# Performance work log

Hardware: AMD Instinct MI355X
Metric: run time of the kernel (lower is better)

The kernel has to match this reference:

```python
import jax, jax.numpy as jnp
import numpy as np

BLOCK_SIZE = 16
NVFP4_LEVELS = np.array([0.0, 0.5, 1.0, 1.5, 2.0, 3.0, 4.0, 6.0], dtype=np.float32)


def quantize_to_nvfp4(x, block_size=BLOCK_SIZE):
    """NVFP4 fake-quant: per-16-element block, scale = amax/6, round |x| to nearest level."""
    levels = jnp.asarray(NVFP4_LEVELS, dtype=x.dtype)
    orig_shape = x.shape
    xf = x.reshape(-1, block_size)                                   # [nblk, 16]
    amax = jnp.clip(jnp.max(jnp.abs(xf), axis=-1, keepdims=True), 1e-12)
    scale = amax / 6.0                                               # [nblk, 1]
    x_norm = jnp.abs(xf) / scale                                     # in [0, 6]
    idx = jnp.argmin(jnp.abs(x_norm[..., None] - levels), axis=-1)   # nearest level (first on ties, like torch)
    x_q = jnp.sign(xf) * levels[idx] * scale
    return x_q.reshape(orig_shape)


def _magnitude_mask_2_4(w):
    # keep 2 largest-|.| of every group of 4 along in_features (row-wise 2:4)
    out_f, in_f = w.shape
    a = jnp.abs(w).reshape(out_f, in_f // 4, 4)
    thr = jnp.sort(a, axis=-1)[..., 2:3]          # 2nd-largest magnitude in group
    mask = (a >= thr).reshape(out_f, in_f)
    return mask.astype(w.dtype)


def setup_inputs() -> dict:
    key = jax.random.key(0)
    k_x, k_w, k_s, k_a, k_b, k_bias = jax.random.split(key, 6)
    B, S, IN_F, OUT_F, RANK = 2, 2048, 4096, 4096, 32
    x = jax.random.normal(k_x, (B, S, IN_F), dtype=jnp.float32)
    smooth_scale = jax.random.uniform(k_s, (IN_F,), dtype=jnp.float32, minval=0.5, maxval=2.0)
    # realistic calibrated weight: 2:4 magnitude-sparse then NVFP4 fake-quantized
    w = jax.random.normal(k_w, (OUT_F, IN_F), dtype=jnp.float32) * 0.02
    w_sparse = w * _magnitude_mask_2_4(w)
    w_quantized = quantize_to_nvfp4(w_sparse)
    lora_a = jax.random.normal(k_a, (RANK, IN_F), dtype=jnp.float32) * 0.02
    lora_b = jax.random.normal(k_b, (OUT_F, RANK), dtype=jnp.float32) * 0.02
    bias = jax.random.normal(k_bias, (OUT_F,), dtype=jnp.float32)
    return {"x": x, "smooth_scale": smooth_scale, "w_quantized": w_quantized,
            "lora_a": lora_a, "lora_b": lora_b, "bias": bias}


def reference(x, smooth_scale, w_quantized, lora_a, lora_b, bias):
    # x: [B, S, IN], smooth_scale: [IN], w_quantized: [OUT, IN]
    x_smoothed = x * smooth_scale                                    # SmoothQuant activation scaling
    x_q = quantize_to_nvfp4(x_smoothed, BLOCK_SIZE)                  # block fake-quant of activations
    base_out = jnp.einsum('bsi,oi->bso', x_q, w_quantized)           # 2:4-sparse quantized matmul
    svd_out = jnp.einsum('bsr,or->bso',
                         jnp.einsum('bsi,ri->bsr', x_smoothed, lora_a), lora_b)  # low-rank correction
    return base_out + svd_out + bias
```

## Files before the change

kernel.cpp:

```cpp
#include <hip/hip_runtime.h>
#include <hip/hip_bf16.h>
#include <stdint.h>

typedef __attribute__((ext_vector_type(8)))  __bf16 bf16x8;
typedef __attribute__((ext_vector_type(4)))  float  f32x4;
typedef __attribute__((ext_vector_type(16))) float  f32x16;

#define KP 4160

__device__ inline void async_copy16(const void* g, void* l) {
  __builtin_amdgcn_global_load_lds((const __attribute__((address_space(1))) void*)g,
                                   (__attribute__((address_space(3))) void*)l, 16, 0, 0);
}

__global__ __launch_bounds__(256) void prep_kernel(
    const float* __restrict__ x, const float* __restrict__ ss,
    const float* __restrict__ w, const float* __restrict__ la,
    const float* __restrict__ lb, __bf16* __restrict__ Ab,
    __bf16* __restrict__ Bb) {
  __shared__ float red[4][16][32];
  int b   = blockIdx.x;
  int tid = threadIdx.x;

  if (b < 2048) {
    int m0 = (b >> 3) << 4;
    int by = b & 7;
    int row = m0 + (tid >> 4);
    int cb0 = tid & 15;
#pragma unroll
    for (int i = 0; i < 2; i++) {
      int col = (by << 9) + ((cb0 + (i << 4)) << 4);
      const float4* xp = (const float4*)(x + ((size_t)row << 12) + col);
      const float4* sp = (const float4*)(ss + col);
      float xs[16];
#pragma unroll
      for (int j = 0; j < 4; j++) {
        float4 xv = xp[j]; float4 sv = sp[j];
        xs[4*j+0] = xv.x * sv.x; xs[4*j+1] = xv.y * sv.y;
        xs[4*j+2] = xv.z * sv.z; xs[4*j+3] = xv.w * sv.w;
      }
      float amax = 0.f;
#pragma unroll
      for (int j = 0; j < 16; j++) amax = fmaxf(amax, fabsf(xs[j]));
      amax = fmaxf(amax, 1e-12f);
      float scale = amax / 6.0f;
      bf16x8 o0, o1;
#pragma unroll
      for (int j = 0; j < 16; j++) {
        float a  = fabsf(xs[j]);
        float xn = a / scale;
        float lvl;
        if (xn < 2.25f) {
          lvl = 0.5f * __builtin_ceilf(__builtin_fmaf(2.0f, xn, -0.5f));
        } else {
          lvl = (xn <= 2.5f) ? 2.0f : (xn <= 3.5f) ? 3.0f
              : (xn <= 5.0f) ? 4.0f : 6.0f;
        }
        float mag = lvl * scale;
        float q = (xs[j] > 0.f) ? mag : ((xs[j] < 0.f) ? -mag : 0.f);
        if (j < 8) o0[j] = (__bf16)q; else o1[j-8] = (__bf16)q;
      }
      __bf16* dst = Ab + (size_t)row * KP + col;
      *(bf16x8*)dst = o0;
      *(bf16x8*)(dst + 8) = o1;
    }
  } else if (b < 10368) {
    int id  = (b - 2048) * 256 + tid;
    int row = id / 520;
    int g   = id - row * 520;
    bf16x8 v;
    if (g < 512) {
      const float4* wp = (const float4*)(w + ((size_t)row << 12) + (g << 3));
      float4 a = wp[0], bb = wp[1];
      v[0]=(__bf16)a.x;  v[1]=(__bf16)a.y;  v[2]=(__bf16)a.z;  v[3]=(__bf16)a.w;
      v[4]=(__bf16)bb.x; v[5]=(__bf16)bb.y; v[6]=(__bf16)bb.z; v[7]=(__bf16)bb.w;
    } else if (g < 516) {
      const float* p = lb + (size_t)row * 32 + ((g - 512) << 3);
#pragma unroll
      for (int j = 0; j < 8; j++) v[j] = (__bf16)p[j];
    } else {
#pragma unroll
      for (int j = 0; j < 8; j++) v[j] = (__bf16)0.f;
    }
    *(bf16x8*)(Bb + (size_t)row * KP + ((size_t)g << 3)) = v;
  } else {
    int j16  = (b - 10368) << 4;
    int wave = tid >> 6, lane = tid & 63;
    int lrow = lane & 15, kg = lane >> 4;
    f32x4 acc0 = {0.f,0.f,0.f,0.f}, acc1 = {0.f,0.f,0.f,0.f};
    const float* xrow = x + ((size_t)(j16 + lrow) << 12);
    const float* a0   = la + ((size_t)lrow << 12);
    const float* a1   = a0 + (16 << 12);
#pragma unroll 4
    for (int k0 = 0; k0 < 32; k0++) {
      int kk = (wave << 10) + (k0 << 5) + (kg << 3);
      float xv[8], sv[8], v0[8], v1[8];
      *(float4*)&xv[0] = *(const float4*)(xrow + kk);
      *(float4*)&xv[4] = *(const float4*)(xrow + kk + 4);
      *(float4*)&sv[0] = *(const float4*)(ss + kk);
      *(float4*)&sv[4] = *(const float4*)(ss + kk + 4);
      *(float4*)&v0[0] = *(const float4*)(a0 + kk);
      *(float4*)&v0[4] = *(const float4*)(a0 + kk + 4);
      *(float4*)&v1[0] = *(const float4*)(a1 + kk);
      *(float4*)&v1[4] = *(const float4*)(a1 + kk + 4);
      bf16x8 af, b0, b1;
#pragma unroll
      for (int q = 0; q < 8; q++) {
        af[q] = (__bf16)(xv[q] * sv[q]);
        b0[q] = (__bf16)v0[q];
        b1[q] = (__bf16)v1[q];
      }
      acc0 = __builtin_amdgcn_mfma_f32_16x16x32_bf16(af, b0, acc0, 0, 0, 0);
      acc1 = __builtin_amdgcn_mfma_f32_16x16x32_bf16(af, b1, acc1, 0, 0, 0);
    }
#pragma unroll
    for (int r = 0; r < 4; r++) {
      red[wave][kg*4 + r][lrow]      = acc0[r];
      red[wave][kg*4 + r][16 + lrow] = acc1[r];
    }
    __syncthreads();
    for (int o = tid; o < 512; o += 256) {
      int rr = o >> 5, cc = o & 31;
      float s = red[0][rr][cc] + red[1][rr][cc] + red[2][rr][cc] + red[3][rr][cc];
      __bf16* dst = Ab + (size_t)(j16 + rr) * KP + 4096;
      dst[cc]      = (__bf16)s;
      dst[32 + cc] = (__bf16)0.f;
    }
  }
}

#define GBAR() __builtin_amdgcn_s_barrier()
#define PRI1() __builtin_amdgcn_s_setprio(1)
#define PRI0() __builtin_amdgcn_s_setprio(0)
#define WVM(n) asm volatile("s_waitcnt vmcnt(" #n ")" ::: "memory")

#define STG(srcb, dstb, bb, h, t) do {                                         \
    const __bf16* _s = (srcb) + (size_t)(h) * (128 * (size_t)KP)               \
                              + ((size_t)(t) << 6);                            \
    char* _d = (dstb) + ((bb) << 15) + ((h) << 14);                            \
    async_copy16(_s, _d);                                                      \
    async_copy16(_s + 32, _d + 1024);                                          \
  } while (0)

#define KOFF(KS) ((((KS) >> 1) << 10) + ((((KS) & 1) << 5) ^ sx))

#define RD_A(base, KS) do { _Pragma("unroll")                                  \
  for (int mf = 0; mf < 4; mf++)                                               \
    af[mf] = *(const bf16x8*)((base) + (mf << 12) + KOFF(KS)); } while (0)

#define RD_B(base, KS) do {                                                    \
    Br[0*4 + (KS)] = *(const bf16x8*)((base) + KOFF(KS));                      \
    Br[1*4 + (KS)] = *(const bf16x8*)((base) + 4096 + KOFF(KS)); } while (0)

#define MM8(KS) do { _Pragma("unroll")                                         \
  for (int mf = 0; mf < 4; mf++) _Pragma("unroll")                             \
  for (int nf = 0; nf < 2; nf++)                                               \
    acc[mf][nf] = __builtin_amdgcn_mfma_f32_32x32x16_bf16(                     \
        af[mf], Br[nf*4 + (KS)], acc[mf][nf], 0, 0, 0); } while (0)

__global__ __launch_bounds__(512, 2) void gemm_kernel(const __bf16* __restrict__ A,
                                                      const __bf16* __restrict__ B,
                                                      const float* __restrict__ bias,
                                                      float* __restrict__ C) {
  extern __shared__ char lds[];
  const int tid  = threadIdx.x;
  const int w    = tid >> 6, lane = tid & 63;
  const int ln31 = lane & 31, kg2 = lane >> 5;
  const int wm   = w >> 2, wn = w & 3;
  const int bid  = blockIdx.x;
  const int sbid = ((bid & 7) << 5) | (bid >> 3);
  const int bm   = sbid >> 4, bn = sbid & 15;
  const size_t m0 = (size_t)bm << 8, n0 = (size_t)bn << 8;

  const int rr = (w << 4) + (lane >> 2);
  const int kk = ((lane & 3) ^ (((lane >> 5) & 1) << 1)) << 3;
  const __bf16* aS = A + (m0 + rr) * (size_t)KP + kk;
  const __bf16* bS = B + (n0 + rr) * (size_t)KP + kk;
  char* dA = lds + (w << 11);
  char* dB = lds + 65536 + (w << 11);

  const int sx = (lane & 8) << 2;
  const int cA = ((ln31 >> 4) << 11) + ((ln31 & 15) << 6) + (kg2 << 4);
  const int cB = ((((wn & 1) << 2) + (ln31 >> 4)) << 11)
               + ((ln31 & 15) << 6) + (kg2 << 4);
  const char* pA0 = lds + (wm << 14) + cA;
  const char* pA1 = pA0 + 32768;
  const char* pB0 = lds + 65536 + ((wn >> 1) << 14) + cB;
  const char* pB1 = pB0 + 32768;

  bf16x8 af[4], Br[8];
  f32x16 acc[4][2];
#pragma unroll
  for (int i = 0; i < 4; i++)
#pragma unroll
    for (int j = 0; j < 2; j++)
#pragma unroll
      for (int q = 0; q < 16; q++) acc[i][j][q] = 0.f;

  STG(bS, dB, 0, 0, 0); STG(bS, dB, 0, 1, 0);
  STG(aS, dA, 0, 0, 0); STG(aS, dA, 0, 1, 0);
  STG(bS, dB, 1, 0, 1); STG(bS, dB, 1, 1, 1);
  WVM(4);
  GBAR();

#pragma unroll 1
  for (int i = 0; i < 32; i++) {
    const int t1 = 2*i + 1, t2 = 2*i + 2;
    int t3 = 2*i + 3; if (t3 > 64) t3 = 64;
    STG(aS, dA, 1, 0, t1);
    RD_B(pB0, 0); RD_B(pB0, 1); RD_A(pA0, 0);
    PRI1(); MM8(0); PRI0();
    GBAR();
    STG(aS, dA, 1, 1, t1);
    RD_B(pB0, 2); RD_B(pB0, 3); RD_A(pA0, 1);
    PRI1(); MM8(1); PRI0();
    GBAR();
    STG(bS, dB, 0, 0, t2);
    RD_A(pA0, 2);
    PRI1(); MM8(2); PRI0();
    GBAR();
    STG(bS, dB, 0, 1, t2);
    RD_A(pA0, 3);
    PRI1(); MM8(3); PRI0();
    WVM(4);
    GBAR();
    STG(aS, dA, 0, 0, t2);
    RD_B(pB1, 0); RD_B(pB1, 1); RD_A(pA1, 0);
    PRI1(); MM8(0); PRI0();
    GBAR();
    STG(aS, dA, 0, 1, t2);
    RD_B(pB1, 2); RD_B(pB1, 3); RD_A(pA1, 1);
    PRI1(); MM8(1); PRI0();
    GBAR();
    STG(bS, dB, 1, 0, t3);
    RD_A(pA1, 2);
    PRI1(); MM8(2); PRI0();
    GBAR();
    STG(bS, dB, 1, 1, t3);
    RD_A(pA1, 3);
    PRI1(); MM8(3); PRI0();
    WVM(4);
    GBAR();
  }

  RD_B(pB0, 0); RD_B(pB0, 1); RD_B(pB0, 2); RD_B(pB0, 3);
  RD_A(pA0, 0); PRI1(); MM8(0); PRI0();
  RD_A(pA0, 1); PRI1(); MM8(1); PRI0();
  RD_A(pA0, 2); PRI1(); MM8(2); PRI0();
  RD_A(pA0, 3); PRI1(); MM8(3); PRI0();

  const int    colb = (int)n0 + (wn << 6) + ln31;
  const size_t rowb = m0 + ((size_t)wm << 7) + (kg2 << 2);
#pragma unroll
  for (int nf = 0; nf < 2; nf++) {
    const int col = colb + (nf << 5);
    const float bv = bias[col];
#pragma unroll
    for (int mf = 0; mf < 4; mf++) {
      const size_t r0 = rowb + ((size_t)mf << 5);
#pragma unroll
      for (int q = 0; q < 16; q++) {
        const size_t row = r0 + (q & 3) + ((q >> 2) << 3);
        C[row * 4096 + col] = acc[mf][nf][q] + bv;
      }
    }
  }
}

extern "C" void kernel_launch(void* const* d_in, const int* in_sizes, int n_in,
                              void* d_out, int out_size, void* d_ws, size_t ws_size,
                              hipStream_t stream) {
  const float* x    = (const float*)d_in[0];
  const float* ss   = (const float*)d_in[1];
  const float* w    = (const float*)d_in[2];
  const float* la   = (const float*)d_in[3];
  const float* lb   = (const float*)d_in[4];
  const float* bias = (const float*)d_in[5];
  float* out = (float*)d_out;

  __bf16* Ab = (__bf16*)d_ws;
  __bf16* Bb = Ab + (size_t)4096 * KP;

  static bool s_attr = false;
  if (!s_attr) {
    hipFuncSetAttribute((const void*)gemm_kernel,
                        hipFuncAttributeMaxDynamicSharedMemorySize, 131072);
    s_attr = true;
  }

  prep_kernel<<<10624, 256, 0, stream>>>(x, ss, w, la, lb, Ab, Bb);
  gemm_kernel<<<256, 512, 131072, stream>>>(Ab, Bb, bias, out);
}
```

Measured before the change: 369.1 us.

## Fuse activation quantization with LoRA-A projection to reuse x reads

The x-quantization blocks now also compute partial LoRA-A products over their 512-column K slice, so each x tile is read once for both uses instead of twice. Partial sums go to a scratch buffer (aliased onto the output), and a second kernel reduces them into the GEMM's extra K columns alongside the weight bf16 conversion. This adds a third launch and a small partial-sum round trip through global memory.

```diff
diff --git a/kernel.cpp b/kernel.cpp
--- a/kernel.cpp
+++ b/kernel.cpp
@@ -13,18 +13,16 @@
                                    (__attribute__((address_space(3))) void*)l, 16, 0, 0);
 }
 
-__global__ __launch_bounds__(256) void prep_kernel(
+__global__ __launch_bounds__(256) void fused_quant_lora_kernel(
     const float* __restrict__ x, const float* __restrict__ ss,
-    const float* __restrict__ w, const float* __restrict__ la,
-    const float* __restrict__ lb, __bf16* __restrict__ Ab,
-    __bf16* __restrict__ Bb) {
+    const float* __restrict__ la, __bf16* __restrict__ Ab,
+    float* __restrict__ Tp) {
   __shared__ float red[4][16][32];
-  int b   = blockIdx.x;
-  int tid = threadIdx.x;
-
-  if (b < 2048) {
-    int m0 = (b >> 3) << 4;
-    int by = b & 7;
+  int tid  = threadIdx.x;
+  int m0   = blockIdx.x << 4;
+  int by   = blockIdx.y;
+
+  {
     int row = m0 + (tid >> 4);
     int cb0 = tid & 15;
 #pragma unroll
@@ -64,8 +62,60 @@
       *(bf16x8*)dst = o0;
       *(bf16x8*)(dst + 8) = o1;
     }
-  } else if (b < 10368) {
-    int id  = (b - 2048) * 256 + tid;
+  }
+
+  {
+    int wave = tid >> 6, lane = tid & 63;
+    int lrow = lane & 15, kg = lane >> 4;
+    int kbase = (by << 9) + (wave << 7);
+    f32x4 acc0 = {0.f,0.f,0.f,0.f}, acc1 = {0.f,0.f,0.f,0.f};
+    const float* xrow = x + ((size_t)(m0 + lrow) << 12);
+    const float* a0   = la + ((size_t)lrow << 12);
+    const float* a1   = a0 + (16 << 12);
+#pragma unroll
+    for (int k0 = 0; k0 < 128; k0 += 32) {
+      int kk = kbase + k0 + (kg << 3);
+      float xv[8], sv[8], v0[8], v1[8];
+      *(float4*)&xv[0] = *(const float4*)(xrow + kk);
+      *(float4*)&xv[4] = *(const float4*)(xrow + kk + 4);
+      *(float4*)&sv[0] = *(const float4*)(ss + kk);
+      *(float4*)&sv[4] = *(const float4*)(ss + kk + 4);
+      *(float4*)&v0[0] = *(const float4*)(a0 + kk);
+      *(float4*)&v0[4] = *(const float4*)(a0 + kk + 4);
+      *(float4*)&v1[0] = *(const float4*)(a1 + kk);
+      *(float4*)&v1[4] = *(const float4*)(a1 + kk + 4);
+      bf16x8 af, b0, b1;
+#pragma unroll
+      for (int j = 0; j < 8; j++) {
+        af[j] = (__bf16)(xv[j] * sv[j]);
+        b0[j] = (__bf16)v0[j];
+        b1[j] = (__bf16)v1[j];
+      }
+      acc0 = __builtin_amdgcn_mfma_f32_16x16x32_bf16(af, b0, acc0, 0, 0, 0);
+      acc1 = __builtin_amdgcn_mfma_f32_16x16x32_bf16(af, b1, acc1, 0, 0, 0);
+    }
+#pragma unroll
+    for (int r = 0; r < 4; r++) {
+      red[wave][kg*4 + r][lrow]      = acc0[r];
+      red[wave][kg*4 + r][16 + lrow] = acc1[r];
+    }
+    __syncthreads();
+    for (int o = tid; o < 512; o += 256) {
+      int rr = o >> 5, cc = o & 31;
+      float s = red[0][rr][cc] + red[1][rr][cc] + red[2][rr][cc] + red[3][rr][cc];
+      Tp[((size_t)by * 4096 + m0 + rr) * 32 + cc] = s;
+    }
+  }
+}
+
+__global__ __launch_bounds__(256) void wconv_fix_kernel(const float* __restrict__ w,
+                                                        const float* __restrict__ lb,
+                                                        const float* __restrict__ Tp,
+                                                        __bf16* __restrict__ Bb,
+                                                        __bf16* __restrict__ Ab) {
+  int b = blockIdx.x;
+  if (b < 8320) {
+    int id  = b * 256 + threadIdx.x;
     int row = id / 520;
     int g   = id - row * 520;
     bf16x8 v;
@@ -84,48 +134,15 @@
     }
     *(bf16x8*)(Bb + (size_t)row * KP + ((size_t)g << 3)) = v;
   } else {
-    int j16  = (b - 10368) << 4;
-    int wave = tid >> 6, lane = tid & 63;
-    int lrow = lane & 15, kg = lane >> 4;
-    f32x4 acc0 = {0.f,0.f,0.f,0.f}, acc1 = {0.f,0.f,0.f,0.f};
-    const float* xrow = x + ((size_t)(j16 + lrow) << 12);
-    const float* a0   = la + ((size_t)lrow << 12);
-    const float* a1   = a0 + (16 << 12);
-#pragma unroll 4
-    for (int k0 = 0; k0 < 32; k0++) {
-      int kk = (wave << 10) + (k0 << 5) + (kg << 3);
-      float xv[8], sv[8], v0[8], v1[8];
-      *(float4*)&xv[0] = *(const float4*)(xrow + kk);
-      *(float4*)&xv[4] = *(const float4*)(xrow + kk + 4);
-      *(float4*)&sv[0] = *(const float4*)(ss + kk);
-      *(float4*)&sv[4] = *(const float4*)(ss + kk + 4);
-      *(float4*)&v0[0] = *(const float4*)(a0 + kk);
-      *(float4*)&v0[4] = *(const float4*)(a0 + kk + 4);
-      *(float4*)&v1[0] = *(const float4*)(a1 + kk);
-      *(float4*)&v1[4] = *(const float4*)(a1 + kk + 4);
-      bf16x8 af, b0, b1;
-#pragma unroll
-      for (int q = 0; q < 8; q++) {
-        af[q] = (__bf16)(xv[q] * sv[q]);
-        b0[q] = (__bf16)v0[q];
-        b1[q] = (__bf16)v1[q];
-      }
-      acc0 = __builtin_amdgcn_mfma_f32_16x16x32_bf16(af, b0, acc0, 0, 0, 0);
-      acc1 = __builtin_amdgcn_mfma_f32_16x16x32_bf16(af, b1, acc1, 0, 0, 0);
-    }
-#pragma unroll
-    for (int r = 0; r < 4; r++) {
-      red[wave][kg*4 + r][lrow]      = acc0[r];
-      red[wave][kg*4 + r][16 + lrow] = acc1[r];
-    }
-    __syncthreads();
-    for (int o = tid; o < 512; o += 256) {
-      int rr = o >> 5, cc = o & 31;
-      float s = red[0][rr][cc] + red[1][rr][cc] + red[2][rr][cc] + red[3][rr][cc];
-      __bf16* dst = Ab + (size_t)(j16 + rr) * KP + 4096;
-      dst[cc]      = (__bf16)s;
-      dst[32 + cc] = (__bf16)0.f;
-    }
+    int id  = (b - 8320) * 256 + threadIdx.x;
+    int row = id >> 5, cc = id & 31;
+    float s = 0.f;
+#pragma unroll
+    for (int kc = 0; kc < 8; kc++)
+      s += Tp[((size_t)kc * 4096 + row) * 32 + cc];
+    __bf16* dst = Ab + (size_t)row * KP + 4096;
+    dst[cc]      = (__bf16)s;
+    dst[32 + cc] = (__bf16)0.f;
   }
 }
 
@@ -280,6 +297,7 @@
 
   __bf16* Ab = (__bf16*)d_ws;
   __bf16* Bb = Ab + (size_t)4096 * KP;
+  float* Tp = out;
 
   static bool s_attr = false;
   if (!s_attr) {
@@ -288,6 +306,7 @@
     s_attr = true;
   }
 
-  prep_kernel<<<10624, 256, 0, stream>>>(x, ss, w, la, lb, Ab, Bb);
+  fused_quant_lora_kernel<<<dim3(256, 8), 256, 0, stream>>>(x, ss, la, Ab, Tp);
+  wconv_fix_kernel<<<8832, 256, 0, stream>>>(w, lb, Tp, Bb, Ab);
   gemm_kernel<<<256, 512, 131072, stream>>>(Ab, Bb, bias, out);
 }
```

Result: faster. 315.4 us (-14.5%).
